# Performance work log

Hardware: AMD Instinct MI355X
Metric: run time of the kernel (lower is better)

The kernel has to match this reference:

```python
import jax, jax.numpy as jnp
import numpy as np

B, S, D, DFF = 8, 2048, 1024, 4096

def setup_inputs() -> dict:
    key = jax.random.key(0)
    ks = jax.random.split(key, 11)
    s = 0.02
    return {
        "x":  jax.random.normal(ks[0], (B, S, D), dtype=jnp.float32),
        "Wq": jax.random.normal(ks[1], (D, D), dtype=jnp.float32) * s,
        "bq": jnp.zeros((D,), dtype=jnp.float32),
        "Wk": jax.random.normal(ks[2], (D, D), dtype=jnp.float32) * s,
        "bk": jnp.zeros((D,), dtype=jnp.float32),
        "Wv": jax.random.normal(ks[3], (D, D), dtype=jnp.float32) * s,
        "bv": jnp.zeros((D,), dtype=jnp.float32),
        "W1": jax.random.normal(ks[4], (DFF, D), dtype=jnp.float32) * s,
        "b1": jnp.zeros((DFF,), dtype=jnp.float32),
        "W2": jax.random.normal(ks[5], (D, DFF), dtype=jnp.float32) * s,
        "b2": jnp.zeros((D,), dtype=jnp.float32),
    }

def reference(x, Wq, bq, Wk, bk, Wv, bv, W1, b1, W2, b2):
    # qkv projections (torch Linear: x @ W.T + b)
    q = jnp.einsum('bsd,ed->bse', x, Wq) + bq
    k = jnp.einsum('bsd,ed->bse', x, Wk) + bk
    v = jnp.einsum('bsd,ed->bse', x, Wv) + bv
    # single-head scaled dot-product attention with causal mask (decoder=True)
    scale = 1.0 / jnp.sqrt(jnp.asarray(q.shape[-1], q.dtype))
    scores = jnp.einsum('bqd,bkd->bqk', q, k) * scale  # (B,S,S)
    causal = jnp.tril(jnp.ones((scores.shape[-2], scores.shape[-1]), dtype=bool))
    scores = jnp.where(causal, scores, jnp.asarray(-jnp.inf, scores.dtype))
    attn = jax.nn.softmax(scores, axis=-1)
    attn_out = jnp.einsum('bqk,bkd->bqd', attn, v)
    # MLP: linear_2(gelu(linear_1(.)))  — exact (erf) GELU as in torch default
    h = jax.nn.gelu(jnp.einsum('bsd,fd->bsf', attn_out, W1) + b1, approximate=False)
    return jnp.einsum('bsf,df->bsd', h, W2) + b2
```

## Files before the change

### kernel.cpp

```cpp
#include <hip/hip_runtime.h>
#include <hip/hip_bf16.h>

#define NB   8
#define SS   2048
#define DD   1024
#define DFFN 4096
#define MTOT (NB*SS)

typedef unsigned short u16;
typedef __attribute__((ext_vector_type(4))) float f32x4;
typedef __attribute__((ext_vector_type(8))) short bf16x8;
typedef __attribute__((ext_vector_type(4))) int i32x4;
typedef __attribute__((ext_vector_type(4))) unsigned short u16x4;
typedef __attribute__((ext_vector_type(8))) unsigned short u16x8;

__device__ __forceinline__ u16 f2bf(float f) {
  union { float f; unsigned u; } c; c.f = f;
  unsigned r = c.u + 0x7FFFu + ((c.u >> 16) & 1u);
  return (u16)(r >> 16);
}

__device__ __forceinline__ void gload16(const void* g, void* l) {
  __builtin_amdgcn_global_load_lds(
      (const __attribute__((address_space(1))) void*)(unsigned long long)g,
      (__attribute__((address_space(3))) void*)(unsigned)(unsigned long long)l,
      16, 0, 0);
}

__device__ __forceinline__ bf16x8 dsr128(unsigned addr) {
  i32x4 r;
  asm volatile("ds_read_b128 %0, %1" : "=v"(r) : "v"(addr));
  return __builtin_bit_cast(bf16x8, r);
}

template<int EBIAS, int EGELU, int ESCALE, int EROWSCALE, int OUTMODE, int CSKIP, int CK>
__global__ __launch_bounds__(256, 4)
void gemm128(const u16* __restrict__ A, const u16* __restrict__ B,
             const float* __restrict__ bias0, const float* __restrict__ bias1,
             const float* __restrict__ bias2, const float* __restrict__ rowscale,
             void* __restrict__ C0, void* __restrict__ C1, void* __restrict__ C2,
             int K, int lda, int ldb, int ldc, float scale,
             long long sA, long long sB, long long sC, int sRS)
{
  __shared__ __align__(1024) u16 smem[16384];

  const int nwg = gridDim.x * gridDim.y;
  const int orig = blockIdx.y * gridDim.x + blockIdx.x;
  const int q = nwg >> 3, r = nwg & 7;
  const int xcd = orig & 7, pos0 = orig >> 3;
  const int wg = (xcd < r ? xcd * (q + 1) : r * (q + 1) + (xcd - r) * q) + pos0;
  const int bx = wg % gridDim.x, by = wg / gridDim.x;
  const int row0 = by * 128, col0 = bx * 128;
  if (CSKIP && col0 > row0 + 127) return;

  const int z = blockIdx.z;
  A += (size_t)z * sA;
  B += (size_t)z * sB;

  int nkt = K >> 5;
  if (CK) { int lim = (row0 + 128) >> 5; if (lim < nkt) nkt = lim; }

  const int tid  = threadIdx.x;
  const int wid  = tid >> 6;
  const int lane = tid & 63;
  const int wr = wid >> 1, wc = wid & 1;

  const int srow = wid * 16 + (lane >> 2);
  const int sunit = (lane & 3) ^ ((lane >> 3) & 3);
  const char* gA = (const char*)A + ((size_t)(row0 + srow) * lda + sunit * 8) * 2;
  const char* gB = (const char*)B + ((size_t)(col0 + srow) * ldb + sunit * 8) * 2;
  const size_t ldab = (size_t)64 * lda * 2;
  const size_t ldbb = (size_t)64 * ldb * 2;

  #define STG(t2) { char* lb = (char*)smem + ((t2) & 1) * 16384; size_t kb = (size_t)(t2) * 64; \
      gload16(gA + kb,        lb + wid * 1024);                                                 \
      gload16(gA + kb + ldab, lb + 4096 + wid * 1024);                                          \
      gload16(gB + kb,        lb + 8192 + wid * 1024);                                          \
      gload16(gB + kb + ldbb, lb + 8192 + 4096 + wid * 1024); }

  const int fr = lane & 15;
  const int ks16 = ((lane >> 4) & 3) * 16;
  const int xm = ((lane >> 1) & 3) << 4;
  const unsigned sbase = (unsigned)(unsigned long long)(void*)smem;

  f32x4 acc[4][4] = {};

  STG(0);
  asm volatile("s_waitcnt vmcnt(0)");
  asm volatile("s_barrier" ::: "memory");

  for (int t = 0; t < nkt; ++t) {
    if (t + 1 < nkt) STG(t + 1);
    const unsigned cb = sbase + (t & 1) * 16384;
    bf16x8 af[4], bf[4];
#pragma unroll
    for (int m = 0; m < 4; ++m)
      af[m] = dsr128(cb + (((wr * 64 + m * 16 + fr) * 64 + ks16) ^ xm));
#pragma unroll
    for (int n = 0; n < 4; ++n)
      bf[n] = dsr128(cb + ((8192 + (wc * 64 + n * 16 + fr) * 64 + ks16) ^ xm));
    asm volatile("s_waitcnt lgkmcnt(0)");
    __builtin_amdgcn_sched_barrier(0);
    __builtin_amdgcn_s_setprio(1);
#pragma unroll
    for (int m = 0; m < 4; ++m)
#pragma unroll
      for (int n = 0; n < 4; ++n)
        acc[m][n] = __builtin_amdgcn_mfma_f32_16x16x32_bf16(af[m], bf[n], acc[m][n], 0, 0, 0);
    __builtin_amdgcn_s_setprio(0);
    asm volatile("s_waitcnt vmcnt(0)");
    asm volatile("s_barrier" ::: "memory");
  }
  #undef STG

  char* sm = (char*)smem;
  const int r4 = (lane >> 4) * 4;
  const int sel  = (OUTMODE == 3) ? (col0 >> 10) : 0;
  const int oc0  = (OUTMODE == 3) ? (col0 & 1023) : col0;
  const float* bias = (OUTMODE == 3) ? (sel == 0 ? bias0 : sel == 1 ? bias1 : bias2)
                                     : bias0;

  if (OUTMODE == 1) {
#pragma unroll
    for (int p = 0; p < 2; ++p) {
      if (wc == p) {
#pragma unroll
        for (int n = 0; n < 4; ++n) {
          const int col = oc0 + wc * 64 + n * 16 + fr;
          const int pb = (n * 16 + fr) * 4;
          float bia = EBIAS ? bias[col] : 0.0f;
#pragma unroll
          for (int m = 0; m < 4; ++m) {
#pragma unroll
            for (int j = 0; j < 4; ++j) {
              const int line = wr * 64 + m * 16 + r4 + j;
              float xv = acc[m][n][j];
              if (EBIAS)     xv += bia;
              if (ESCALE)    xv *= scale;
              if (EROWSCALE) xv *= rowscale[z * sRS + row0 + line];
              if (EGELU)     xv = 0.5f * xv * (1.0f + erff(xv * 0.70710678118f));
              *(float*)(sm + ((line * 256 + pb) ^ ((line & 7) << 4))) = xv;
            }
          }
        }
      }
      __syncthreads();
      float* Cb = (float*)C0 + (size_t)z * sC;
#pragma unroll
      for (int i = 0; i < 8; ++i) {
        const int o = i * 4096 + tid * 16;
        const int line = o >> 8, ps = o & 255;
        f32x4 v = *(const f32x4*)(sm + ((line * 256 + ps) ^ ((line & 7) << 4)));
        *(f32x4*)((char*)(Cb + (size_t)(row0 + line) * ldc + oc0 + p * 64) + ps) = v;
      }
      __syncthreads();
    }
  } else if (OUTMODE == 3 && sel == 2) {
#pragma unroll
    for (int n = 0; n < 4; ++n) {
      const int line = wc * 64 + n * 16 + fr;
      float bia = EBIAS ? bias[oc0 + line] : 0.0f;
#pragma unroll
      for (int m = 0; m < 4; ++m) {
        const int rb = wr * 64 + m * 16 + r4;
        u16x4 pk;
#pragma unroll
        for (int j = 0; j < 4; ++j) pk[j] = f2bf(acc[m][n][j] + bia);
        *(u16x4*)(sm + ((line * 256 + rb * 2) ^ ((line & 7) << 4))) = pk;
      }
    }
    __syncthreads();
    u16* Cb = (u16*)C2 + (size_t)(row0 >> 11) * (DD * SS) + (row0 & (SS - 1));
#pragma unroll
    for (int i = 0; i < 8; ++i) {
      const int o = i * 4096 + tid * 16;
      const int line = o >> 8, ps = o & 255;
      f32x4 v = *(const f32x4*)(sm + ((line * 256 + ps) ^ ((line & 7) << 4)));
      *(f32x4*)((char*)(Cb + (size_t)(oc0 + line) * SS) + ps) = v;
    }
  } else {
#pragma unroll
    for (int n = 0; n < 4; ++n) {
      const int col = oc0 + wc * 64 + n * 16 + fr;
      const int pc = (wc * 64 + n * 16 + fr) * 2;
      float bia = EBIAS ? bias[col] : 0.0f;
#pragma unroll
      for (int m = 0; m < 4; ++m) {
#pragma unroll
        for (int j = 0; j < 4; ++j) {
          const int line = wr * 64 + m * 16 + r4 + j;
          float xv = acc[m][n][j];
          if (EBIAS)     xv += bia;
          if (ESCALE)    xv *= scale;
          if (EROWSCALE) xv *= rowscale[z * sRS + row0 + line];
          if (EGELU)     xv = 0.5f * xv * (1.0f + erff(xv * 0.70710678118f));
          u16 u;
          if (OUTMODE == 2) { union { u16 s; _Float16 h; } cu; cu.h = (_Float16)xv; u = cu.s; }
          else u = f2bf(xv);
          *(u16*)(sm + ((line * 256 + pc) ^ ((line & 7) << 4))) = u;
        }
      }
    }
    __syncthreads();
    u16* Cb = (u16*)(OUTMODE == 3 ? (sel ? C1 : C0) : C0) + (size_t)z * sC + oc0;
#pragma unroll
    for (int i = 0; i < 8; ++i) {
      const int o = i * 4096 + tid * 16;
      const int line = o >> 8, ps = o & 255;
      f32x4 v = *(const f32x4*)(sm + ((line * 256 + ps) ^ ((line & 7) << 4)));
      *(f32x4*)((char*)(Cb + (size_t)(row0 + line) * ldc) + ps) = v;
    }
  }
}

__global__ __launch_bounds__(256) void cvt_all_k(
    const float* __restrict__ x,  const float* __restrict__ wq,
    const float* __restrict__ wk, const float* __restrict__ wv,
    const float* __restrict__ w1, const float* __restrict__ w2,
    u16* __restrict__ out_x, u16* __restrict__ out_w)
{
  const int i = blockIdx.x * 256 + threadIdx.x;
  const float* src; int off; u16* dst; int dofs;
  if (i < 4194304)      { src = x;  off = i;           dst = out_x; dofs = i; }
  else if (i < 4456448) { src = wq; off = i - 4194304; dst = out_w; dofs = i - 4194304; }
  else if (i < 4718592) { src = wk; off = i - 4456448; dst = out_w; dofs = i - 4194304; }
  else if (i < 4980736) { src = wv; off = i - 4718592; dst = out_w; dofs = i - 4194304; }
  else if (i < 6029312) { src = w1; off = i - 4980736; dst = out_w; dofs = i - 4194304; }
  else                  { src = w2; off = i - 6029312; dst = out_w; dofs = i - 4194304; }
  float4 v = ((const float4*)src)[off];
  u16x4 o;
  o.x = f2bf(v.x); o.y = f2bf(v.y); o.z = f2bf(v.z); o.w = f2bf(v.w);
  ((u16x4*)dst)[dofs] = o;
}

__global__ __launch_bounds__(256) void softmax_k(u16* __restrict__ sc, float* __restrict__ rinv, int rows0) {
  const int widx = blockIdx.x * 4 + (threadIdx.x >> 6);
  const int lane = threadIdx.x & 63;
  u16* row = sc + (size_t)widx * SS;
  const int L = (widx & (SS - 1)) + 1;
  float mx = -1e30f;
  for (int k = 0; k < 4; ++k) {
    const int j0 = k * 512 + lane * 8;
    if (j0 < L) {
      u16x8 v = *(const u16x8*)(row + j0);
      int lim = L - j0; if (lim > 8) lim = 8;
#pragma unroll
      for (int e = 0; e < 8; ++e) {
        if (e < lim) { union { u16 u; _Float16 h; } c; c.u = v[e]; mx = fmaxf(mx, (float)c.h); }
      }
    }
  }
#pragma unroll
  for (int o = 32; o >= 1; o >>= 1) mx = fmaxf(mx, __shfl_xor(mx, o));
  float s = 0.0f;
  for (int k = 0; k < 4; ++k) {
    const int j0 = k * 512 + lane * 8;
    u16x8 v = *(const u16x8*)(row + j0);
    u16x8 w;
#pragma unroll
    for (int e = 0; e < 8; ++e) {
      const int j = j0 + e;
      float ev = 0.0f;
      if (j < L) { union { u16 u; _Float16 h; } c; c.u = v[e]; ev = __expf((float)c.h - mx); s += ev; }
      w[e] = f2bf(ev);
    }
    *(u16x8*)(row + j0) = w;
  }
#pragma unroll
  for (int o = 32; o >= 1; o >>= 1) s += __shfl_xor(s, o);
  if (lane == 0) rinv[rows0 + widx] = 1.0f / s;
}

extern "C" void kernel_launch(void* const* d_in, const int* in_sizes, int n_in,
                              void* d_out, int out_size, void* d_ws, size_t ws_size,
                              hipStream_t stream) {
  const float* x  = (const float*)d_in[0];
  const float* Wq = (const float*)d_in[1];
  const float* bq = (const float*)d_in[2];
  const float* Wk = (const float*)d_in[3];
  const float* bk = (const float*)d_in[4];
  const float* Wv = (const float*)d_in[5];
  const float* bv = (const float*)d_in[6];
  const float* W1 = (const float*)d_in[7];
  const float* b1 = (const float*)d_in[8];
  const float* W2 = (const float*)d_in[9];
  const float* b2 = (const float*)d_in[10];

  char* ws = (char*)d_ws;
  const int big8 = (ws_size >= 190906368ull);
  const int GB = big8 ? 8 : 4;
  const int MC = big8 ? 16384 : 8192;

  u16*  Qb   = (u16*)(ws);
  u16*  Kb   = (u16*)(ws + 33554432);
  u16*  Vtb  = (u16*)(ws + 67108864);
  u16*  big  = (u16*)(ws + 100663296);
  const size_t woff = 100663296ull + (size_t)GB * 8388608ull;
  float* rinv = (float*)(ws + woff);
  u16*  Wcat = (u16*)(ws + woff + 65536);
  u16*  W1b  = Wcat + 3 * DD * DD;
  u16*  W2b  = W1b + DFFN * DD;
  u16*  xb   = big;
  u16*  att  = Qb;
  u16*  h    = Kb;

  cvt_all_k<<<27648, 256, 0, stream>>>(x, Wq, Wk, Wv, W1, W2, xb, Wcat);

  gemm128<1,0,0,0,3,0,0><<<dim3(3 * DD / 128, MTOT / 128), 256, 0, stream>>>(
      xb, Wcat, bq, bk, bv, nullptr, (void*)Qb, (void*)Kb, (void*)Vtb,
      DD, DD, DD, DD, 0.f, 0, 0, 0, 0);

  for (int b0 = 0; b0 < NB; b0 += GB) {
    gemm128<0,0,1,0,2,1,0><<<dim3(SS/128, SS/128, GB), 256, 0, stream>>>(
        Qb + (size_t)b0 * SS * DD, Kb + (size_t)b0 * SS * DD,
        nullptr, nullptr, nullptr, nullptr, (void*)big, nullptr, nullptr,
        DD, DD, DD, SS, 0.03125f,
        (long long)SS * DD, (long long)SS * DD, (long long)SS * SS, 0);
    softmax_k<<<GB * SS / 4, 256, 0, stream>>>(big, rinv, b0 * SS);
    gemm128<0,0,0,1,0,0,1><<<dim3(DD/128, SS/128, GB), 256, 0, stream>>>(
        big, Vtb + (size_t)b0 * DD * SS,
        nullptr, nullptr, nullptr, rinv + (size_t)b0 * SS,
        (void*)(att + (size_t)b0 * SS * DD), nullptr, nullptr,
        SS, SS, SS, DD, 0.f,
        (long long)SS * SS, (long long)DD * SS, (long long)SS * DD, SS);
  }

  for (int c = 0; c < MTOT / MC; ++c) {
    gemm128<1,1,0,0,0,0,0><<<dim3(DFFN/128, MC/128), 256, 0, stream>>>(
        att + (size_t)c * MC * DD, W1b, b1, nullptr, nullptr, nullptr,
        (void*)h, nullptr, nullptr,
        DD, DD, DD, DFFN, 0.f, 0, 0, 0, 0);
    gemm128<1,0,0,0,1,0,0><<<dim3(DD/128, MC/128), 256, 0, stream>>>(
        h, W2b, b2, nullptr, nullptr, nullptr,
        (void*)((float*)d_out + (size_t)c * MC * DD), nullptr, nullptr,
        DFFN, DFFN, DFFN, DD, 0.f, 0, 0, 0, 0);
  }
}
```

Baseline: 701.6 us.

## Add 256x256 phased MFMA GEMM for MLP and drop workspace-size chunking

Adds a new 512-thread GEMM kernel with 256x256 tiles, double-buffered LDS (128KB), XCD-aware block remapping and interleaved global-to-LDS loads with MFMA phases. The kernel handles both MLP layers, with GELU fused into the first and fp32 output with bias in the second. The workspace-size-dependent batching is removed, so attention and the MLP run as single full-size launches. Larger tiles raise data reuse and cut launch count, but the code now assumes a large workspace, and the big LDS footprint limits occupancy.

```diff
diff --git a/kernel.cpp b/kernel.cpp
--- a/kernel.cpp
+++ b/kernel.cpp
@@ -209,6 +209,178 @@
       const int line = o >> 8, ps = o & 255;
       f32x4 v = *(const f32x4*)(sm + ((line * 256 + ps) ^ ((line & 7) << 4)));
       *(f32x4*)((char*)(Cb + (size_t)(row0 + line) * ldc) + ps) = v;
+    }
+  }
+}
+
+template<int EGELU, int OUTF32>
+__global__ __launch_bounds__(512, 2)
+void gemm256ph(const u16* __restrict__ A, const u16* __restrict__ B,
+               const float* __restrict__ bias, void* __restrict__ C,
+               int K, int lda, int ldb, int ldc)
+{
+  __shared__ __align__(1024) u16 smem[65536];
+
+  const int nwg = gridDim.x * gridDim.y;
+  const int orig = blockIdx.y * gridDim.x + blockIdx.x;
+  const int q = nwg >> 3, r = nwg & 7;
+  const int xcd = orig & 7, pos0 = orig >> 3;
+  const int wg = (xcd < r ? xcd * (q + 1) : r * (q + 1) + (xcd - r) * q) + pos0;
+  const int bx = wg % gridDim.x, by = wg / gridDim.x;
+  const int row0 = by * 256, col0 = bx * 256;
+
+  const int nkt = K >> 6;
+  const int tid = threadIdx.x, wid = tid >> 6, lane = tid & 63;
+  const int wr = wid >> 2, wc = wid & 3;
+  const int fr = lane & 15, s = lane >> 4;
+
+  const unsigned aoff0 = wr * 16384 + fr * 128 + (((s)     ^ (fr & 7)) << 4);
+  const unsigned aoff1 = wr * 16384 + fr * 128 + (((4 + s) ^ (fr & 7)) << 4);
+  const unsigned boff0 = 32768 + wc * 8192 + fr * 128 + (((s)     ^ (fr & 7)) << 4);
+  const unsigned boff1 = 32768 + wc * 8192 + fr * 128 + (((4 + s) ^ (fr & 7)) << 4);
+  const unsigned sb = (unsigned)(unsigned long long)(void*)smem;
+
+  const int l8 = lane >> 3;
+  const int u8 = (lane & 7) ^ (l8 & 7);
+  const char* gAl = (const char*)A + ((size_t)(row0 + wid * 8 + l8) * lda) * 2 + u8 * 16;
+  const char* gBl = (const char*)B + ((size_t)(col0 + wid * 8 + l8) * ldb) * 2 + u8 * 16;
+  const size_t lda64 = (size_t)64 * lda * 2;
+  const size_t ldb64 = (size_t)64 * ldb * 2;
+
+  #define STGA(BUFB, S4, TT) gload16(gAl + (S4) * lda64 + (size_t)(TT) * 128, \
+      (char*)smem + (BUFB) + ((S4) * 64 + wid * 8) * 128)
+  #define STGB(BUFB, S4, TT) gload16(gBl + (S4) * ldb64 + (size_t)(TT) * 128, \
+      (char*)smem + (BUFB) + 32768 + ((S4) * 64 + wid * 8) * 128)
+
+  #define RDA(BUFB, M0) {                                        \
+    av[0] = dsr128(sb + (BUFB) + (M0) * 2048 + aoff0);           \
+    av[1] = dsr128(sb + (BUFB) + (M0) * 2048 + aoff1);           \
+    av[2] = dsr128(sb + (BUFB) + ((M0) + 1) * 2048 + aoff0);     \
+    av[3] = dsr128(sb + (BUFB) + ((M0) + 1) * 2048 + aoff1); }
+  #define RDB(BUFB) {                                            \
+    _Pragma("unroll") for (int n = 0; n < 4; ++n) {              \
+      bb[n * 2]     = dsr128(sb + (BUFB) + n * 2048 + boff0);    \
+      bb[n * 2 + 1] = dsr128(sb + (BUFB) + n * 2048 + boff1); } }
+
+  f32x4 acc[8][4] = {};
+  bf16x8 av[4], bb[8];
+
+  #define MFMA16(P)                                                            \
+    __builtin_amdgcn_s_setprio(1);                                             \
+    _Pragma("unroll") for (int mm = 0; mm < 2; ++mm)                           \
+    _Pragma("unroll") for (int n = 0; n < 4; ++n)                              \
+    _Pragma("unroll") for (int h = 0; h < 2; ++h)                              \
+      acc[(P) * 2 + mm][n] = __builtin_amdgcn_mfma_f32_16x16x32_bf16(          \
+          av[mm * 2 + h], bb[n * 2 + h], acc[(P) * 2 + mm][n], 0, 0, 0);       \
+    __builtin_amdgcn_s_setprio(0);
+
+  #define BAR       asm volatile("s_barrier" ::: "memory")
+  #define LGK0      asm volatile("s_waitcnt lgkmcnt(0)" ::: "memory"); \
+                    __builtin_amdgcn_sched_barrier(0)
+
+  STGB(0, 0, 0); STGB(0, 1, 0); STGB(0, 2, 0); STGB(0, 3, 0);
+  STGA(0, 0, 0); STGA(0, 1, 0); STGA(0, 2, 0); STGA(0, 3, 0);
+  asm volatile("s_waitcnt vmcnt(0)" ::: "memory");
+  BAR;
+
+  for (int T = 0; T < nkt - 1; ++T) {
+    const unsigned cb = (unsigned)(T & 1) * 65536u;
+    const unsigned nb = cb ^ 65536u;
+    RDB(cb); RDA(cb, 0);
+    STGB(nb, 0, T + 1); STGB(nb, 1, T + 1);
+    BAR; LGK0; MFMA16(0); BAR;
+    RDA(cb, 2);
+    STGB(nb, 2, T + 1); STGB(nb, 3, T + 1);
+    asm volatile("s_waitcnt vmcnt(4)" ::: "memory");
+    BAR; LGK0; MFMA16(1); BAR;
+    RDA(cb, 4);
+    STGA(nb, 0, T + 1); STGA(nb, 2, T + 1);
+    BAR; LGK0; MFMA16(2); BAR;
+    RDA(cb, 6);
+    STGA(nb, 1, T + 1); STGA(nb, 3, T + 1);
+    asm volatile("s_waitcnt vmcnt(2)" ::: "memory");
+    BAR; LGK0; MFMA16(3); BAR;
+  }
+  {
+    const unsigned cb = (unsigned)((nkt - 1) & 1) * 65536u;
+    RDB(cb); RDA(cb, 0);
+    BAR; LGK0; MFMA16(0); BAR;
+    RDA(cb, 2);
+    asm volatile("s_waitcnt vmcnt(0)" ::: "memory");
+    BAR; LGK0; MFMA16(1); BAR;
+    RDA(cb, 4);
+    BAR; LGK0; MFMA16(2); BAR;
+    RDA(cb, 6);
+    BAR; LGK0; MFMA16(3); BAR;
+  }
+  #undef STGA
+  #undef STGB
+  #undef RDA
+  #undef RDB
+  #undef MFMA16
+  #undef BAR
+  #undef LGK0
+
+  __syncthreads();
+
+  char* sm = (char*)smem;
+  const int r4 = s * 4;
+
+  if (OUTF32) {
+#pragma unroll
+    for (int p = 0; p < 2; ++p) {
+      if ((wc >> 1) == p) {
+#pragma unroll
+        for (int n = 0; n < 4; ++n) {
+          const int col = col0 + wc * 64 + n * 16 + fr;
+          const int pb = ((wc & 1) * 64 + n * 16 + fr) * 4;
+          const float bia = bias[col];
+#pragma unroll
+          for (int m = 0; m < 8; ++m) {
+#pragma unroll
+            for (int j = 0; j < 4; ++j) {
+              const int line = wr * 128 + m * 16 + r4 + j;
+              float xv = acc[m][n][j] + bia;
+              if (EGELU) xv = 0.5f * xv * (1.0f + erff(xv * 0.70710678118f));
+              *(float*)(sm + ((line * 512 + pb) ^ ((line & 7) << 4))) = xv;
+            }
+          }
+        }
+      }
+      __syncthreads();
+#pragma unroll
+      for (int i = 0; i < 16; ++i) {
+        const int o = i * 8192 + tid * 16;
+        const int line = o >> 9, ps = o & 511;
+        f32x4 v = *(const f32x4*)(sm + ((line * 512 + ps) ^ ((line & 7) << 4)));
+        *(f32x4*)((char*)((float*)C + (size_t)(row0 + line) * ldc + col0 + p * 128) + ps) = v;
+      }
+      __syncthreads();
+    }
+  } else {
+#pragma unroll
+    for (int n = 0; n < 4; ++n) {
+      const int col = col0 + wc * 64 + n * 16 + fr;
+      const int pc = (wc * 64 + n * 16 + fr) * 2;
+      const float bia = bias[col];
+#pragma unroll
+      for (int m = 0; m < 8; ++m) {
+#pragma unroll
+        for (int j = 0; j < 4; ++j) {
+          const int line = wr * 128 + m * 16 + r4 + j;
+          float xv = acc[m][n][j] + bia;
+          if (EGELU) xv = 0.5f * xv * (1.0f + erff(xv * 0.70710678118f));
+          *(u16*)(sm + ((line * 512 + pc) ^ ((line & 7) << 4))) = f2bf(xv);
+        }
+      }
+    }
+    __syncthreads();
+#pragma unroll
+    for (int i = 0; i < 16; ++i) {
+      const int o = i * 8192 + tid * 16;
+      const int line = o >> 9, ps = o & 511;
+      f32x4 v = *(const f32x4*)(sm + ((line * 512 + ps) ^ ((line & 7) << 4)));
+      *(f32x4*)((char*)((u16*)C + (size_t)(row0 + line) * ldc + col0) + ps) = v;
     }
   }
 }
@@ -252,7 +424,7 @@
   }
 #pragma unroll
   for (int o = 32; o >= 1; o >>= 1) mx = fmaxf(mx, __shfl_xor(mx, o));
-  float s = 0.0f;
+  float sacc = 0.0f;
   for (int k = 0; k < 4; ++k) {
     const int j0 = k * 512 + lane * 8;
     u16x8 v = *(const u16x8*)(row + j0);
@@ -261,14 +433,14 @@
     for (int e = 0; e < 8; ++e) {
       const int j = j0 + e;
       float ev = 0.0f;
-      if (j < L) { union { u16 u; _Float16 h; } c; c.u = v[e]; ev = __expf((float)c.h - mx); s += ev; }
+      if (j < L) { union { u16 u; _Float16 h; } c; c.u = v[e]; ev = __expf((float)c.h - mx); sacc += ev; }
       w[e] = f2bf(ev);
     }
     *(u16x8*)(row + j0) = w;
   }
 #pragma unroll
-  for (int o = 32; o >= 1; o >>= 1) s += __shfl_xor(s, o);
-  if (lane == 0) rinv[rows0 + widx] = 1.0f / s;
+  for (int o = 32; o >= 1; o >>= 1) sacc += __shfl_xor(sacc, o);
+  if (lane == 0) rinv[rows0 + widx] = 1.0f / sacc;
 }
 
 extern "C" void kernel_launch(void* const* d_in, const int* in_sizes, int n_in,
@@ -287,17 +459,12 @@
   const float* b2 = (const float*)d_in[10];
 
   char* ws = (char*)d_ws;
-  const int big8 = (ws_size >= 190906368ull);
-  const int GB = big8 ? 8 : 4;
-  const int MC = big8 ? 16384 : 8192;
-
   u16*  Qb   = (u16*)(ws);
   u16*  Kb   = (u16*)(ws + 33554432);
   u16*  Vtb  = (u16*)(ws + 67108864);
   u16*  big  = (u16*)(ws + 100663296);
-  const size_t woff = 100663296ull + (size_t)GB * 8388608ull;
-  float* rinv = (float*)(ws + woff);
-  u16*  Wcat = (u16*)(ws + woff + 65536);
+  float* rinv = (float*)(ws + 167772160);
+  u16*  Wcat = (u16*)(ws + 167772160 + 65536);
   u16*  W1b  = Wcat + 3 * DD * DD;
   u16*  W2b  = W1b + DFFN * DD;
   u16*  xb   = big;
@@ -310,29 +477,19 @@
       xb, Wcat, bq, bk, bv, nullptr, (void*)Qb, (void*)Kb, (void*)Vtb,
       DD, DD, DD, DD, 0.f, 0, 0, 0, 0);
 
-  for (int b0 = 0; b0 < NB; b0 += GB) {
-    gemm128<0,0,1,0,2,1,0><<<dim3(SS/128, SS/128, GB), 256, 0, stream>>>(
-        Qb + (size_t)b0 * SS * DD, Kb + (size_t)b0 * SS * DD,
-        nullptr, nullptr, nullptr, nullptr, (void*)big, nullptr, nullptr,
-        DD, DD, DD, SS, 0.03125f,
-        (long long)SS * DD, (long long)SS * DD, (long long)SS * SS, 0);
-    softmax_k<<<GB * SS / 4, 256, 0, stream>>>(big, rinv, b0 * SS);
-    gemm128<0,0,0,1,0,0,1><<<dim3(DD/128, SS/128, GB), 256, 0, stream>>>(
-        big, Vtb + (size_t)b0 * DD * SS,
-        nullptr, nullptr, nullptr, rinv + (size_t)b0 * SS,
-        (void*)(att + (size_t)b0 * SS * DD), nullptr, nullptr,
-        SS, SS, SS, DD, 0.f,
-        (long long)SS * SS, (long long)DD * SS, (long long)SS * DD, SS);
-  }
-
-  for (int c = 0; c < MTOT / MC; ++c) {
-    gemm128<1,1,0,0,0,0,0><<<dim3(DFFN/128, MC/128), 256, 0, stream>>>(
-        att + (size_t)c * MC * DD, W1b, b1, nullptr, nullptr, nullptr,
-        (void*)h, nullptr, nullptr,
-        DD, DD, DD, DFFN, 0.f, 0, 0, 0, 0);
-    gemm128<1,0,0,0,1,0,0><<<dim3(DD/128, MC/128), 256, 0, stream>>>(
-        h, W2b, b2, nullptr, nullptr, nullptr,
-        (void*)((float*)d_out + (size_t)c * MC * DD), nullptr, nullptr,
-        DFFN, DFFN, DFFN, DD, 0.f, 0, 0, 0, 0);
-  }
-}
+  gemm128<0,0,1,0,2,1,0><<<dim3(SS/128, SS/128, NB), 256, 0, stream>>>(
+      Qb, Kb, nullptr, nullptr, nullptr, nullptr, (void*)big, nullptr, nullptr,
+      DD, DD, DD, SS, 0.03125f,
+      (long long)SS * DD, (long long)SS * DD, (long long)SS * SS, 0);
+  softmax_k<<<NB * SS / 4, 256, 0, stream>>>(big, rinv, 0);
+  gemm128<0,0,0,1,0,0,1><<<dim3(DD/128, SS/128, NB), 256, 0, stream>>>(
+      big, Vtb, nullptr, nullptr, nullptr, rinv,
+      (void*)att, nullptr, nullptr,
+      SS, SS, SS, DD, 0.f,
+      (long long)SS * SS, (long long)DD * SS, (long long)SS * DD, SS);
+
+  gemm256ph<1,0><<<dim3(DFFN/256, MTOT/256), 512, 0, stream>>>(
+      att, W1b, b1, (void*)h, DD, DD, DD, DFFN);
+  gemm256ph<0,1><<<dim3(DD/256, MTOT/256), 512, 0, stream>>>(
+      h, W2b, b2, (void*)d_out, DFFN, DFFN, DFFN, DD);
+}
```

Measured after the change: 713.4 us. No clear change (+1.7%).
